# Optimization experiments

Measured on AMD Instinct MI355X. Metric: run time of the kernel, lower is better.

## Reference

```python
import jax, jax.numpy as jnp
import numpy as np

K = 16          # image_bin
C = 4           # label_bin
BW_CAM = 0.005
BW_LAB = 0.001
BETA = 500.0
EPS_SM = 1e-12
EPS = 1e-07


def setup_inputs() -> dict:
    key = jax.random.key(0)
    k1, k2 = jax.random.split(key)
    camera = jax.random.uniform(k1, (8, 3, 512, 1024), dtype=jnp.float32)
    label = jax.random.normal(k2, (8, 4, 512, 1024), dtype=jnp.float32)
    return {"camera": camera, "label": label}


def _soft_arg_max(A):
    # softmax over channel dim with temperature beta, then expectation of index
    A_max = jnp.max(A, axis=1, keepdims=True)
    A_exp = jnp.exp((A - A_max) * BETA)
    A_softmax = A_exp / (jnp.sum(A_exp, axis=1, keepdims=True) + EPS_SM)
    idx = jnp.arange(A.shape[1], dtype=A.dtype)
    return jnp.einsum('bchw,c->bhw', A_softmax, idx)  # (B,H,W)


def _probabilities(camera_gray, label_amax):
    B, H, W = camera_gray.shape
    N = H * W
    cam = camera_gray.reshape(B, N)    # (B,N)
    lab = label_amax.reshape(B, N)     # (B,N)

    L_c = 1.0 / K
    mu_c = L_c * (jnp.arange(K, dtype=cam.dtype) + 0.5)      # (K,)
    dc = cam[None, :, :] - mu_c[:, None, None]               # (K,B,N)
    PI_c = jax.nn.sigmoid((dc + L_c / 2) / BW_CAM) - jax.nn.sigmoid((dc - L_c / 2) / BW_CAM)
    P_c = jnp.sum(PI_c, axis=1)                              # (K,N)

    mu_l = jnp.arange(C, dtype=lab.dtype)                    # (C,) bin centers at k, width 1
    dl = lab[None, :, :] - mu_l[:, None, None]               # (C,B,N)
    PI_l = jax.nn.sigmoid((dl + 0.5) / BW_LAB) - jax.nn.sigmoid((dl - 0.5) / BW_LAB)
    P_l = jnp.sum(PI_l, axis=1)                              # (C,N)

    norm = N * B
    p_cl = (P_c @ P_l.T) / norm      # (K,C)
    p_c = jnp.sum(P_c, axis=1) / norm  # (K,)
    p_l = jnp.sum(P_l, axis=1) / norm  # (C,)
    return p_cl, p_c, p_l


def reference(camera, label):
    camera_gray = jnp.sum(camera, axis=1) / 3.0              # (B,H,W)
    label_amax = _soft_arg_max(label)                        # (B,H,W)
    p_cl, p_c, p_l = _probabilities(camera_gray, label_amax)
    p_cl = p_cl / jnp.sum(p_cl)
    p_c = p_c / jnp.sum(p_c)
    p_l = p_l / jnp.sum(p_l)
    outer = p_c[:, None] * p_l[None, :]                      # (K,C)
    log_pcl = jnp.log(p_cl + EPS)
    I = jnp.sum(p_cl * (log_pcl - jnp.log(outer + EPS)))
    H_ent = -jnp.sum(p_cl * log_pcl)
    nid = 1.0 - I / H_ent
    return (nid - 0.95) * 20.0
```

## Files before the change

### kernel.cpp

```cpp
#include <hip/hip_runtime.h>
#include <math.h>

#define NPIX (512*1024)
#define NB   8
#define KBINS 16
#define CBINS 4
#define NACC 68
#define BLOCKS 1024
#define TPB 256
#define HROWS 20
#define HCOLS 512

__device__ __forceinline__ float fexp2(float x){ return __builtin_amdgcn_exp2f(x); }
__device__ __forceinline__ float frcp (float x){ return __builtin_amdgcn_rcpf(x); }

__device__ __forceinline__ void camWin(float gsum, float* __restrict__ colbase)
{
    constexpr float L2E  = 1.4426950408889634f;
    constexpr float ESTP = 12.5f * L2E;
    float u  = gsum * (16.0f / 3.0f);
    float jr = rintf(u);
    float d  = u - jr;
    int   ji = (int)jr;
    float em = fexp2(fmaf(d, -ESTP, -ESTP));
    float ep = fexp2(fmaf(d,  ESTP, -ESTP));
    float s0 = frcp(1.0f + fexp2(-ESTP * d));
    float* p = colbase + ji * HCOLS;
    p[0 * HCOLS] += em;
    p[1 * HCOLS] += 1.0f - em - s0;
    p[2 * HCOLS] += s0 - ep;
    p[3 * HCOLS] += ep;
}

__device__ __forceinline__ void labelAccum(float x0, float x1, float x2, float x3,
                                           float (&pl)[CBINS])
{
    constexpr float L2E = 1.4426950408889634f;
    constexpr float BSC = 500.0f * L2E;
    constexpr float LSC = 1000.0f * L2E;
    float m  = fmaxf(fmaxf(x0, x1), fmaxf(x2, x3));
    float mk = m * BSC;
    float e0 = fexp2(fmaf(x0, BSC, -mk));
    float e1 = fexp2(fmaf(x1, BSC, -mk));
    float e2 = fexp2(fmaf(x2, BSC, -mk));
    float e3 = fexp2(fmaf(x3, BSC, -mk));
    float am = fmaf(3.0f, e3, fmaf(2.0f, e2, e1)) * frcp(e0 + e1 + e2 + e3 + 1e-12f);

    float fj = rintf(am + 0.5f);
    float v  = frcp(1.0f + fexp2((fj - 0.5f - am) * LSC));
    #pragma unroll
    for (int c = 0; c < CBINS; c++) {
        float add = (fj == (float)(c + 1)) ? (1.0f - v)
                  : (fj == (float)c)       ? v : 0.0f;
        pl[c] += add;
    }
}

__launch_bounds__(TPB, 4)
__global__ void nid_partial(const float* __restrict__ cam,
                            const float* __restrict__ lab,
                            float* __restrict__ ws)
{
    __shared__ float buf[HROWS * HCOLS];

    const int t   = threadIdx.x;
    const int tid = blockIdx.x * TPB + t;
    const int n0  = tid * 2;

    float* col0 = buf + t;
    float* col1 = buf + 256 + t;

    #pragma unroll
    for (int r = 0; r < HROWS; r++) {
        col0[r * HCOLS] = 0.0f;
        col1[r * HCOLS] = 0.0f;
    }

    float pl0[CBINS] = {0.f, 0.f, 0.f, 0.f};
    float pl1[CBINS] = {0.f, 0.f, 0.f, 0.f};

    #pragma unroll
    for (int b = 0; b < NB; b++) {
        const float* cbase = cam + (size_t)(b * 3) * NPIX + n0;
        float2 c0 = *(const float2*)(cbase);
        float2 c1 = *(const float2*)(cbase + NPIX);
        float2 c2 = *(const float2*)(cbase + 2 * NPIX);
        const float* lbase = lab + (size_t)(b * 4) * NPIX + n0;
        float2 a0 = *(const float2*)(lbase);
        float2 a1 = *(const float2*)(lbase + NPIX);
        float2 a2 = *(const float2*)(lbase + 2 * NPIX);
        float2 a3 = *(const float2*)(lbase + 3 * NPIX);

        camWin(c0.x + c1.x + c2.x, col0);
        camWin(c0.y + c1.y + c2.y, col1);
        labelAccum(a0.x, a1.x, a2.x, a3.x, pl0);
        labelAccum(a0.y, a1.y, a2.y, a3.y, pl1);
    }

    float Pc0[KBINS], Pc1[KBINS];
    #pragma unroll
    for (int k = 0; k < KBINS; k++) {
        Pc0[k] = col0[(k + 2) * HCOLS];
        Pc1[k] = col1[(k + 2) * HCOLS];
    }

    float acc[NACC];
    #pragma unroll
    for (int k = 0; k < KBINS; k++) {
        #pragma unroll
        for (int c = 0; c < CBINS; c++)
            acc[k * 4 + c] = fmaf(Pc0[k], pl0[c], Pc1[k] * pl1[c]);
    }
    #pragma unroll
    for (int c = 0; c < CBINS; c++) acc[64 + c] = pl0[c] + pl1[c];

    __syncthreads();
    float (*red)[NACC] = (float (*)[NACC])buf;
    const int lane = t & 63;
    const int wv   = t >> 6;

    #pragma unroll
    for (int i = 0; i < NACC; i++) {
        float v = acc[i];
        v += __shfl_xor(v, 1);
        v += __shfl_xor(v, 2);
        v += __shfl_xor(v, 4);
        if ((lane & 7) == 0) red[wv * 8 + (lane >> 3)][i] = v;
    }

    __syncthreads();
    if (t < NACC) {
        float s = 0.f;
        #pragma unroll
        for (int g = 0; g < 32; g++) s += red[g][t];
        ws[(size_t)blockIdx.x * NACC + t] = s;
    }
}

__global__ void nid_final(const float* __restrict__ ws, float* __restrict__ out)
{
    __shared__ double partA[8][NACC];
    __shared__ double sm[NACC];
    __shared__ double tots[2];
    const int t = threadIdx.x;

    if (t < 8 * NACC) {
        int v = t % NACC;
        int g = t / NACC;
        double s = 0.0;
        #pragma unroll 8
        for (int i = g * 128; i < g * 128 + 128; i++)
            s += (double)ws[(size_t)i * NACC + v];
        partA[g][v] = s;
    }
    __syncthreads();
    if (t < NACC) {
        double s = 0.0;
        #pragma unroll
        for (int g = 0; g < 8; g++) s += partA[g][t];
        sm[t] = s;
    }
    __syncthreads();
    if (t == 0) {
        double a = 0, bb = 0;
        for (int v = 0; v < 64; v++) a += sm[v];
        for (int c = 0; c < 4; c++)  bb += sm[64 + c];
        tots[0] = a; tots[1] = bb;
    }
    __syncthreads();
    if (t < 64) {
        int k = t >> 2, c = t & 3;
        double pcl = sm[t] / tots[0];
        double pc  = (sm[k * 4] + sm[k * 4 + 1] + sm[k * 4 + 2] + sm[k * 4 + 3]) / tots[0];
        double pll = sm[64 + c] / tots[1];
        double lp  = log(pcl + 1e-7);
        double lo  = log(pc * pll + 1e-7);
        double dI  = pcl * (lp - lo);
        double dH  = -pcl * lp;
        #pragma unroll
        for (int mm = 1; mm < 64; mm <<= 1) {
            dI += __shfl_xor(dI, mm);
            dH += __shfl_xor(dH, mm);
        }
        if (t == 0) out[0] = (float)((1.0 - dI / dH - 0.95) * 20.0);
    }
}

extern "C" void kernel_launch(void* const* d_in, const int* in_sizes, int n_in,
                              void* d_out, int out_size, void* d_ws, size_t ws_size,
                              hipStream_t stream)
{
    const float* cam = (const float*)d_in[0];
    const float* lab = (const float*)d_in[1];
    float* ws = (float*)d_ws;

    hipLaunchKernelGGL(nid_partial, dim3(BLOCKS), dim3(TPB), 0, stream, cam, lab, ws);
    hipLaunchKernelGGL(nid_final, dim3(1), dim3(544), 0, stream, ws, (float*)d_out);
}
```

Before: 41.75 us.

## Stage inputs through LDS with async global_load_lds triple buffering

```diff
diff --git a/kernel.cpp b/kernel.cpp
--- a/kernel.cpp
+++ b/kernel.cpp
@@ -8,13 +8,15 @@
 #define NACC 68
 #define BLOCKS 1024
 #define TPB 256
-#define HROWS 20
+#define PXB 512
+#define HROWS 18
 #define HCOLS 512
+#define SBUF (7*512)
 
 __device__ __forceinline__ float fexp2(float x){ return __builtin_amdgcn_exp2f(x); }
 __device__ __forceinline__ float frcp (float x){ return __builtin_amdgcn_rcpf(x); }
 
-__device__ __forceinline__ void camWin(float gsum, float* __restrict__ colbase)
+__device__ __forceinline__ void camWin(float gsum, float* __restrict__ col)
 {
     constexpr float L2E  = 1.4426950408889634f;
     constexpr float ESTP = 12.5f * L2E;
@@ -25,11 +27,12 @@
     float em = fexp2(fmaf(d, -ESTP, -ESTP));
     float ep = fexp2(fmaf(d,  ESTP, -ESTP));
     float s0 = frcp(1.0f + fexp2(-ESTP * d));
-    float* p = colbase + ji * HCOLS;
-    p[0 * HCOLS] += em;
-    p[1 * HCOLS] += 1.0f - em - s0;
-    p[2 * HCOLS] += s0 - ep;
-    p[3 * HCOLS] += ep;
+    int r2 = (ji <= 15) ? ji + 2 : ji - 16;
+    int r3 = (ji <= 14) ? ji + 3 : ji - 15;
+    col[ji * HCOLS]       += em;
+    col[(ji + 1) * HCOLS] += 1.0f - em - s0;
+    col[r2 * HCOLS]       += s0 - ep;
+    col[r3 * HCOLS]       += ep;
 }
 
 __device__ __forceinline__ void labelAccum(float x0, float x1, float x2, float x3,
@@ -56,52 +59,77 @@
     }
 }
 
-__launch_bounds__(TPB, 4)
+__launch_bounds__(TPB, 2)
 __global__ void nid_partial(const float* __restrict__ cam,
                             const float* __restrict__ lab,
                             float* __restrict__ ws)
 {
-    __shared__ float buf[HROWS * HCOLS];
-
-    const int t   = threadIdx.x;
-    const int tid = blockIdx.x * TPB + t;
-    const int n0  = tid * 2;
-
-    float* col0 = buf + t;
-    float* col1 = buf + 256 + t;
+    __shared__ float stage[3][SBUF];
+    __shared__ float hist[HROWS * HCOLS];
+
+    const int t  = threadIdx.x;
+    const int nb = blockIdx.x * PXB;
 
     #pragma unroll
     for (int r = 0; r < HROWS; r++) {
-        col0[r * HCOLS] = 0.0f;
-        col1[r * HCOLS] = 0.0f;
-    }
+        hist[r * HCOLS + t]       = 0.0f;
+        hist[r * HCOLS + 256 + t] = 0.0f;
+    }
+
+    auto STAGE = [&](int b, int buf) {
+        #pragma unroll
+        for (int i = 0; i < 4; i++) {
+            int c  = (i < 3) ? (t + 256 * i) : (768 + (t & 127));
+            int pl = c >> 7;
+            int w  = c & 127;
+            const float* src = (pl < 3)
+                ? cam + (size_t)(b * 3 + pl) * NPIX + nb + w * 4
+                : lab + (size_t)(b * 4 + (pl - 3)) * NPIX + nb + w * 4;
+            __builtin_amdgcn_global_load_lds(
+                (const __attribute__((address_space(1))) void*)src,
+                (__attribute__((address_space(3))) void*)&stage[buf][c * 4],
+                16, 0, 0);
+        }
+    };
 
     float pl0[CBINS] = {0.f, 0.f, 0.f, 0.f};
     float pl1[CBINS] = {0.f, 0.f, 0.f, 0.f};
 
+    STAGE(0, 0);
+    STAGE(1, 1);
+
     #pragma unroll
     for (int b = 0; b < NB; b++) {
-        const float* cbase = cam + (size_t)(b * 3) * NPIX + n0;
-        float2 c0 = *(const float2*)(cbase);
-        float2 c1 = *(const float2*)(cbase + NPIX);
-        float2 c2 = *(const float2*)(cbase + 2 * NPIX);
-        const float* lbase = lab + (size_t)(b * 4) * NPIX + n0;
-        float2 a0 = *(const float2*)(lbase);
-        float2 a1 = *(const float2*)(lbase + NPIX);
-        float2 a2 = *(const float2*)(lbase + 2 * NPIX);
-        float2 a3 = *(const float2*)(lbase + 3 * NPIX);
-
-        camWin(c0.x + c1.x + c2.x, col0);
-        camWin(c0.y + c1.y + c2.y, col1);
-        labelAccum(a0.x, a1.x, a2.x, a3.x, pl0);
-        labelAccum(a0.y, a1.y, a2.y, a3.y, pl1);
+        if (b + 2 < NB) {
+            STAGE(b + 2, (b + 2) % 3);
+            asm volatile("s_waitcnt vmcnt(8)" ::: "memory");
+        } else if (b + 1 < NB) {
+            asm volatile("s_waitcnt vmcnt(4)" ::: "memory");
+        } else {
+            asm volatile("s_waitcnt vmcnt(0)" ::: "memory");
+        }
+        __builtin_amdgcn_s_barrier();
+        __builtin_amdgcn_sched_barrier(0);
+
+        const float* sb = stage[b % 3];
+        float g0 = sb[0 * 512 + t] + sb[1 * 512 + t] + sb[2 * 512 + t];
+        float g1 = sb[0 * 512 + 256 + t] + sb[1 * 512 + 256 + t] + sb[2 * 512 + 256 + t];
+        camWin(g0, hist + t);
+        camWin(g1, hist + 256 + t);
+        labelAccum(sb[3 * 512 + t], sb[4 * 512 + t],
+                   sb[5 * 512 + t], sb[6 * 512 + t], pl0);
+        labelAccum(sb[3 * 512 + 256 + t], sb[4 * 512 + 256 + t],
+                   sb[5 * 512 + 256 + t], sb[6 * 512 + 256 + t], pl1);
+
+        __builtin_amdgcn_sched_barrier(0);
+        __builtin_amdgcn_s_barrier();
     }
 
     float Pc0[KBINS], Pc1[KBINS];
     #pragma unroll
     for (int k = 0; k < KBINS; k++) {
-        Pc0[k] = col0[(k + 2) * HCOLS];
-        Pc1[k] = col1[(k + 2) * HCOLS];
+        Pc0[k] = hist[(k + 2) * HCOLS + t];
+        Pc1[k] = hist[(k + 2) * HCOLS + 256 + t];
     }
 
     float acc[NACC];
@@ -115,7 +143,7 @@
     for (int c = 0; c < CBINS; c++) acc[64 + c] = pl0[c] + pl1[c];
 
     __syncthreads();
-    float (*red)[NACC] = (float (*)[NACC])buf;
+    float (*red)[NACC] = (float (*)[NACC])hist;
     const int lane = t & 63;
     const int wv   = t >> 6;
 
```

Result: slower. 50.40 us (+20.7%).
